# Kernel tuning notes

Measured on AMD Instinct MI355X. Metric: run time of the kernel, lower is better.

Reference implementation:

```python
import jax, jax.numpy as jnp
import numpy as np

N = 100000   # nodes
E = 1000000  # edges (avg degree 10)
F_IN, H1, H2, C = 128, 64, 64, 16


def setup_inputs() -> dict:
    key = jax.random.key(0)
    ks = jax.random.split(key, 10)
    x = jax.random.normal(ks[0], (N, F_IN), dtype=jnp.float32)
    edge_src = jax.random.randint(ks[1], (E,), 0, N, dtype=jnp.int32)
    edge_dst = jax.random.randint(ks[2], (E,), 0, N, dtype=jnp.int32)
    # normalized-adjacency-like positive edge weights (~1/deg scale)
    edge_val = jax.random.uniform(ks[3], (E,), dtype=jnp.float32) * 0.1
    def glorot(k, fan_in, fan_out):
        s = np.float32(1.0 / np.sqrt(fan_in))
        return jax.random.normal(k, (fan_in, fan_out), dtype=jnp.float32) * s
    W1 = glorot(ks[4], F_IN, H1)
    W2 = glorot(ks[5], H1, H2)
    W3 = glorot(ks[6], H2, C)
    b1 = jnp.zeros((H1,), jnp.float32)
    b2 = jnp.zeros((H2,), jnp.float32)
    b3 = jnp.zeros((C,), jnp.float32)
    return {"x": x, "edge_val": edge_val, "W1": W1, "b1": b1,
            "W2": W2, "b2": b2, "W3": W3, "b3": b3,
            "edge_src": edge_src, "edge_dst": edge_dst}


def gcn_layer(h, W, b, edge_src, edge_dst, edge_val):
    # support = h @ W ; out = spmm(adj, support) + b
    support = h @ W                                  # [N, d_out]
    msg = support[edge_src] * edge_val[:, None]      # [E, d_out] gather + scale
    agg = jax.ops.segment_sum(msg, edge_dst, num_segments=N)  # scatter-add
    return agg + b


def reference(x, edge_val, W1, b1, W2, b2, W3, b3, edge_src, edge_dst):
    # eval mode: F.dropout(training=False) is identity
    h = jax.nn.relu(gcn_layer(x, W1, b1, edge_src, edge_dst, edge_val))
    h = jax.nn.relu(gcn_layer(h, W2, b2, edge_src, edge_dst, edge_val))
    return gcn_layer(h, W3, b3, edge_src, edge_dst, edge_val)  # [N, C] logits
```

## Files before the change

### kernel.cpp

```cpp
#include <hip/hip_runtime.h>
#include <stdint.h>

#define N_NODES 100000
#define N_EDGES 1000000
#define NBUCK 196
#define CAP 6656

typedef __attribute__((ext_vector_type(8))) __bf16 bf16x8;
typedef __attribute__((ext_vector_type(4))) float f32x4;

static __device__ __forceinline__ float bf2f(unsigned short u) {
    return __uint_as_float(((unsigned int)u) << 16);
}
static __device__ __forceinline__ unsigned short f2bf(float f) {
    unsigned int u = __float_as_uint(f);
    unsigned int r = (u + 0x7FFFu + ((u >> 16) & 1u)) >> 16;
    return (unsigned short)r;
}
static __device__ __forceinline__ void st8_half(unsigned short* p, const float* f) {
    int4 u;
    u.x = (int)(((unsigned)f2bf(f[0])) | (((unsigned)f2bf(f[1])) << 16));
    u.y = (int)(((unsigned)f2bf(f[2])) | (((unsigned)f2bf(f[3])) << 16));
    u.z = (int)(((unsigned)f2bf(f[4])) | (((unsigned)f2bf(f[5])) << 16));
    u.w = (int)(((unsigned)f2bf(f[6])) | (((unsigned)f2bf(f[7])) << 16));
    *(int4*)p = u;
}

static __device__ __forceinline__ float ldf(const void* p, size_t i, int bf) {
    return bf ? bf2f(((const unsigned short*)p)[i]) : ((const float*)p)[i];
}

__global__ __launch_bounds__(256) void detect_kernel(const unsigned short* __restrict__ xs,
                                                     int* __restrict__ flag,
                                                     int* __restrict__ bcursor) {
    __shared__ int sz;
    if (threadIdx.x == 0) sz = 0;
    __syncthreads();
    int z = 0;
    for (int i = threadIdx.x; i < 1024; i += 256) {
        float av = fabsf(bf2f(xs[2 * i]));
        if (!(av <= 1048576.0f) || (av != 0.0f && av < 9.5367431640625e-07f)) z++;
    }
    atomicAdd(&sz, z);
    if (threadIdx.x < NBUCK) bcursor[threadIdx.x] = threadIdx.x * CAP;
    __syncthreads();
    if (threadIdx.x == 0) *flag = (sz > 256) ? 0 : 1;
}

__global__ __launch_bounds__(256) void part_kernel(const int* __restrict__ src,
                                                   const int* __restrict__ dst,
                                                   const void* __restrict__ val,
                                                   int* __restrict__ bcursor,
                                                   int2* __restrict__ part,
                                                   const int* __restrict__ flagp) {
    __shared__ int cnt[NBUCK];
    __shared__ int base[NBUCK];
    const int bf = *flagp;
    const int tid = threadIdx.x;
    const int e0 = blockIdx.x * 2048;
    for (int i = tid; i < NBUCK; i += 256) cnt[i] = 0;
    __syncthreads();
    int rank[8], bkt[8], pk[8], vb[8];
#pragma unroll
    for (int i = 0; i < 8; ++i) {
        int e = e0 + i * 256 + tid;
        bkt[i] = -1;
        if (e < N_EDGES) {
            int d = dst[e];
            int b = d >> 9;
            bkt[i] = b;
            pk[i] = src[e] | ((d & 511) << 17);
            vb[i] = __float_as_int(ldf(val, e, bf));
            rank[i] = atomicAdd(&cnt[b], 1);
        }
    }
    __syncthreads();
    for (int i = tid; i < NBUCK; i += 256) {
        int c = cnt[i];
        base[i] = c ? atomicAdd(&bcursor[i], c) : 0;
    }
    __syncthreads();
#pragma unroll
    for (int i = 0; i < 8; ++i) {
        if (bkt[i] >= 0) part[(size_t)base[bkt[i]] + rank[i]] = make_int2(pk[i], vb[i]);
    }
}

__global__ __launch_bounds__(512) void place_kernel(const int* __restrict__ bcursor,
                                                    const int2* __restrict__ part,
                                                    int* __restrict__ row_start,
                                                    int2* __restrict__ csr_rec) {
    __shared__ int cnt[512];
    __shared__ int sums[512];
    __shared__ int sh_s, sh_cnt, sh_total;
    const int tid = threadIdx.x;
    const int b = blockIdx.x;
    const int row0 = b << 9;
    const int nrows = min(512, N_NODES - row0);

    if (tid < 256) sums[tid] = (tid < NBUCK) ? (bcursor[tid] - tid * CAP) : 0;
    __syncthreads();
    for (int off = 1; off < 256; off <<= 1) {
        int t = 0;
        if (tid < 256 && tid >= off) t = sums[tid - off];
        __syncthreads();
        if (tid < 256 && tid >= off) sums[tid] += t;
        __syncthreads();
    }
    if (tid == 0) {
        sh_s = (b > 0) ? sums[b - 1] : 0;
        sh_cnt = bcursor[b] - b * CAP;
        sh_total = sums[NBUCK - 1];
    }
    __syncthreads();
    const int s = sh_s;
    const int cb = sh_cnt;
    const int ps = b * CAP;
    const int total = sh_total;

    cnt[tid] = 0;
    __syncthreads();
    for (int j = tid; j < cb; j += 512) {
        unsigned p = (unsigned)part[ps + j].x;
        atomicAdd(&cnt[p >> 17], 1);
    }
    __syncthreads();
    int own = cnt[tid];
    sums[tid] = own;
    __syncthreads();
    for (int off = 1; off < 512; off <<= 1) {
        int t = 0;
        if (tid >= off) t = sums[tid - off];
        __syncthreads();
        if (tid >= off) sums[tid] += t;
        __syncthreads();
    }
    int excl = sums[tid] - own;
    cnt[tid] = s + excl;
    if (tid < nrows) row_start[row0 + tid] = s + excl;
    if (b == NBUCK - 1 && tid == 0) row_start[N_NODES] = total;
    __syncthreads();
    for (int j = tid; j < cb; j += 512) {
        int2 r = part[ps + j];
        unsigned p = (unsigned)r.x;
        int pos = atomicAdd(&cnt[p >> 17], 1);
        csr_rec[pos] = make_int2((int)(p & 0x1FFFFu), r.y);
    }
}

template <int RS>
static __device__ __forceinline__ void row_gather(const unsigned short* __restrict__ supc,
                                                  const int2* __restrict__ csr_rec,
                                                  int s, int e, float a[8]) {
    if (s >= e) return;
    int2 r[4];
#pragma unroll
    for (int t = 0; t < 4; ++t) r[t] = csr_rec[min(s + t, e - 1)];
    for (int j = s; j < e; j += 4) {
        int4 sp[4];
#pragma unroll
        for (int t = 0; t < 4; ++t) sp[t] = *(const int4*)(supc + (size_t)r[t].x * RS);
        float wv[4];
#pragma unroll
        for (int t = 0; t < 4; ++t) wv[t] = (j + t < e) ? __int_as_float(r[t].y) : 0.0f;
        int jn = j + 4;
        if (jn < e) {
#pragma unroll
            for (int t = 0; t < 4; ++t) r[t] = csr_rec[min(jn + t, e - 1)];
        }
#pragma unroll
        for (int t = 0; t < 4; ++t) {
            float w = wv[t];
            int q[4] = {sp[t].x, sp[t].y, sp[t].z, sp[t].w};
#pragma unroll
            for (int c = 0; c < 4; ++c) {
                float flo = __uint_as_float(((unsigned)q[c]) << 16);
                float fhi = __uint_as_float(((unsigned)q[c]) & 0xffff0000u);
                a[2 * c]     += w * flo;
                a[2 * c + 1] += w * fhi;
            }
        }
    }
}

template <int K, int M, bool DYNIN>
__global__ __launch_bounds__(256, 8) void mgemm_kernel(const void* __restrict__ hv_,
                                                       const void* __restrict__ W,
                                                       unsigned short* __restrict__ out,
                                                       const int* __restrict__ flagp) {
    constexpr int KP = K + 8;
    constexpr int NC = M / 16;
    constexpr int NK = K / 32;

    __shared__ unsigned short wt[M][KP];

    const int bf = *flagp;
    const int tid = threadIdx.x;

    for (int i = tid; i < K * M; i += 256) {
        int k = i / M, m = i % M;
        wt[m][k] = f2bf(ldf(W, i, bf));
    }
    __syncthreads();

    const int lane = tid & 63;
    const int qd = lane >> 4;
    const int ln = lane & 15;
    const int wrow = (tid >> 6) * 16;
    const int tile = blockIdx.x;

    const int row = tile * 64 + wrow + ln;
    const bool ok = row < N_NODES;

    f32x4 acc[NC];
#pragma unroll
    for (int c = 0; c < NC; ++c) acc[c] = (f32x4){0.f, 0.f, 0.f, 0.f};

#pragma unroll
    for (int ks = 0; ks < NK; ++ks) {
        bf16x8 a;
        if (ok) {
            const size_t base = (size_t)row * K + ks * 32 + qd * 8;
            if (DYNIN && !bf) {
                const float* xp = (const float*)hv_ + base;
                float4 f0 = *(const float4*)xp;
                float4 f1 = *(const float4*)(xp + 4);
                ushort4 uu[2];
                uu[0].x = f2bf(f0.x); uu[0].y = f2bf(f0.y); uu[0].z = f2bf(f0.z); uu[0].w = f2bf(f0.w);
                uu[1].x = f2bf(f1.x); uu[1].y = f2bf(f1.y); uu[1].z = f2bf(f1.z); uu[1].w = f2bf(f1.w);
                a = *(const bf16x8*)uu;
            } else {
                a = *(const bf16x8*)((const unsigned short*)hv_ + base);
            }
        } else {
            a = (bf16x8)(__bf16)0.0f;
        }
#pragma unroll
        for (int c = 0; c < NC; ++c) {
            bf16x8 b = *(const bf16x8*)&wt[c * 16 + ln][ks * 32 + qd * 8];
            acc[c] = __builtin_amdgcn_mfma_f32_16x16x32_bf16(a, b, acc[c], 0, 0, 0);
        }
    }

#pragma unroll
    for (int c = 0; c < NC; ++c) {
#pragma unroll
        for (int r = 0; r < 4; ++r) {
            int orow = tile * 64 + wrow + qd * 4 + r;
            if (orow < N_NODES) out[(size_t)orow * M + c * 16 + ln] = f2bf(acc[c][r]);
        }
    }
}

template <int MOUT>
__global__ __launch_bounds__(256, 8) void fused_kernel(const unsigned short* __restrict__ support,
                                                       const int* __restrict__ row_start,
                                                       const int2* __restrict__ csr_rec,
                                                       const void* __restrict__ bias,
                                                       const void* __restrict__ W,
                                                       unsigned short* __restrict__ out,
                                                       const int* __restrict__ flagp) {
    constexpr int K = 64, KP = 72;
    constexpr int NC = MOUT / 16;
    constexpr int NK = 2;

    __shared__ unsigned short agg[64][KP];
    __shared__ unsigned short wt[MOUT][KP];

    const int bf = *flagp;
    const int tid = threadIdx.x;

    for (int i = tid; i < K * MOUT; i += 256) {
        int k = i / MOUT, m = i % MOUT;
        wt[m][k] = f2bf(ldf(W, i, bf));
    }

    const int lane = tid & 63;
    const int qd = lane >> 4;
    const int ln = lane & 15;
    const int wrow = (tid >> 6) * 16;

    const int grp = tid >> 3;
    const int cc = tid & 7;
    const unsigned short* supc = support + cc * 8;

    const int tile = blockIdx.x;
    const int rowA = tile * 64 + grp;
    const int rowB = rowA + 32;
    int s0 = row_start[min(rowA, N_NODES)];
    int e0 = row_start[min(rowA + 1, N_NODES)];
    int s1 = row_start[min(rowB, N_NODES)];
    int e1 = row_start[min(rowB + 1, N_NODES)];

    {
        float a[8];
#pragma unroll
        for (int c = 0; c < 8; ++c) a[c] = 0.0f;
        row_gather<64>(supc, csr_rec, s0, e0, a);
#pragma unroll
        for (int c = 0; c < 8; ++c) a[c] = fmaxf(a[c] + ldf(bias, cc * 8 + c, bf), 0.f);
        st8_half(&agg[grp][cc * 8], a);
    }
    {
        float a[8];
#pragma unroll
        for (int c = 0; c < 8; ++c) a[c] = 0.0f;
        row_gather<64>(supc, csr_rec, s1, e1, a);
#pragma unroll
        for (int c = 0; c < 8; ++c) a[c] = fmaxf(a[c] + ldf(bias, cc * 8 + c, bf), 0.f);
        st8_half(&agg[32 + grp][cc * 8], a);
    }
    __syncthreads();

    f32x4 macc[NC];
#pragma unroll
    for (int c = 0; c < NC; ++c) macc[c] = (f32x4){0.f, 0.f, 0.f, 0.f};
#pragma unroll
    for (int ks = 0; ks < NK; ++ks) {
        bf16x8 a = *(const bf16x8*)&agg[wrow + ln][ks * 32 + qd * 8];
#pragma unroll
        for (int c = 0; c < NC; ++c) {
            bf16x8 b = *(const bf16x8*)&wt[c * 16 + ln][ks * 32 + qd * 8];
            macc[c] = __builtin_amdgcn_mfma_f32_16x16x32_bf16(a, b, macc[c], 0, 0, 0);
        }
    }

#pragma unroll
    for (int c = 0; c < NC; ++c) {
#pragma unroll
        for (int r = 0; r < 4; ++r) {
            int orow = tile * 64 + wrow + qd * 4 + r;
            if (orow < N_NODES) out[(size_t)orow * MOUT + c * 16 + ln] = f2bf(macc[c][r]);
        }
    }
}

template <bool DYNOUT>
__global__ __launch_bounds__(256, 8) void spmm16_kernel(const unsigned short* __restrict__ support,
                                                        const int* __restrict__ row_start,
                                                        const int2* __restrict__ csr_rec,
                                                        const void* __restrict__ bias,
                                                        void* __restrict__ out_,
                                                        const int* __restrict__ flagp) {
    constexpr int M = 16;
    int bf = *flagp;
    int tid = threadIdx.x;
    int grp = tid >> 1;
    int cc = tid & 1;
    int row = blockIdx.x * 128 + grp;
    if (row >= N_NODES) return;
    int s = row_start[row];
    int e = row_start[row + 1];
    float a[8];
#pragma unroll
    for (int c = 0; c < 8; ++c) a[c] = 0.0f;
    row_gather<16>(support + cc * 8, csr_rec, s, e, a);
#pragma unroll
    for (int c = 0; c < 8; ++c) a[c] += ldf(bias, cc * 8 + c, bf);
    if (DYNOUT && !bf) {
        float* op = (float*)out_ + (size_t)row * M + cc * 8;
        *(float4*)op = make_float4(a[0], a[1], a[2], a[3]);
        *(float4*)(op + 4) = make_float4(a[4], a[5], a[6], a[7]);
    } else {
        st8_half((unsigned short*)out_ + (size_t)row * M + cc * 8, a);
    }
}

extern "C" void kernel_launch(void* const* d_in, const int* in_sizes, int n_in,
                              void* d_out, int out_size, void* d_ws, size_t ws_size,
                              hipStream_t stream) {
    (void)in_sizes; (void)n_in; (void)out_size; (void)ws_size;
    const void* x  = d_in[0];
    const void* ev = d_in[1];
    const void* W1 = d_in[2];
    const void* b1 = d_in[3];
    const void* W2 = d_in[4];
    const void* b2 = d_in[5];
    const void* W3 = d_in[6];
    const void* b3 = d_in[7];
    const int* esrc = (const int*)d_in[8];
    const int* edst = (const int*)d_in[9];

    char* ws = (char*)d_ws;
    size_t off = 0;
    auto alloc = [&](size_t bytes) -> void* {
        void* p = ws + off;
        off = (off + bytes + 255) & ~(size_t)255;
        return p;
    };
    unsigned short* A = (unsigned short*)alloc((size_t)N_NODES * 64 * 2);
    unsigned short* B = (unsigned short*)alloc((size_t)N_NODES * 64 * 2);
    int* row_start  = (int*)alloc((size_t)(N_NODES + 1) * 4);
    int* bcursor    = (int*)alloc(1024);
    int2* csr_rec   = (int2*)alloc((size_t)N_EDGES * 8);
    int* flagp      = (int*)alloc(256);
    int2* part      = (int2*)A;

    detect_kernel<<<1, 256, 0, stream>>>((const unsigned short*)x, flagp, bcursor);

    part_kernel<<<(N_EDGES + 2047) / 2048, 256, 0, stream>>>(esrc, edst, ev, bcursor, part, flagp);
    place_kernel<<<NBUCK, 512, 0, stream>>>(bcursor, part, row_start, csr_rec);

    const int NT = (N_NODES + 63) / 64;

    mgemm_kernel<128, 64, true><<<NT, 256, 0, stream>>>(x, W1, A, flagp);
    fused_kernel<64><<<NT, 256, 0, stream>>>(A, row_start, csr_rec, b1, W2, B, flagp);
    fused_kernel<16><<<NT, 256, 0, stream>>>(B, row_start, csr_rec, b2, W3, A, flagp);
    spmm16_kernel<true><<<(N_NODES + 127) / 128, 256, 0, stream>>>(A, row_start, csr_rec, b3, d_out, flagp);
}
```

Measured before the change: 228.1 us.

## Balance SpMM gather by splitting tile edges evenly with LDS atomic accumulation

Instead of assigning one destination row per thread group, each block now splits its tile's contiguous edge range evenly across thread groups. Groups accumulate per-row partials in registers and flush them to shared-memory fp32 accumulators with atomics whenever the destination row changes. Bias, ReLU and bf16 conversion move to the MFMA load stage. The gather loop is widened to 8 edges in flight. This targets load imbalance from varying degrees and tail divergence, at the cost of LDS atomics, extra shared memory, and dropped occupancy hints.

```diff
diff --git a/kernel.cpp b/kernel.cpp
--- a/kernel.cpp
+++ b/kernel.cpp
@@ -144,32 +144,47 @@
         int2 r = part[ps + j];
         unsigned p = (unsigned)r.x;
         int pos = atomicAdd(&cnt[p >> 17], 1);
-        csr_rec[pos] = make_int2((int)(p & 0x1FFFFu), r.y);
-    }
-}
-
-template <int RS>
-static __device__ __forceinline__ void row_gather(const unsigned short* __restrict__ supc,
+        csr_rec[pos] = make_int2((int)p, r.y);
+    }
+}
+
+template <int RS, int RMASK, int AST>
+static __device__ __forceinline__ void seg_gather(const unsigned short* __restrict__ supc,
                                                   const int2* __restrict__ csr_rec,
-                                                  int s, int e, float a[8]) {
+                                                  int s, int e,
+                                                  float* __restrict__ aggc ) {
     if (s >= e) return;
-    int2 r[4];
-#pragma unroll
-    for (int t = 0; t < 4; ++t) r[t] = csr_rec[min(s + t, e - 1)];
-    for (int j = s; j < e; j += 4) {
-        int4 sp[4];
-#pragma unroll
-        for (int t = 0; t < 4; ++t) sp[t] = *(const int4*)(supc + (size_t)r[t].x * RS);
-        float wv[4];
-#pragma unroll
-        for (int t = 0; t < 4; ++t) wv[t] = (j + t < e) ? __int_as_float(r[t].y) : 0.0f;
-        int jn = j + 4;
+    int2 r[8];
+#pragma unroll
+    for (int t = 0; t < 8; ++t) r[t] = csr_rec[min(s + t, e - 1)];
+    int cur = (r[0].x >> 17) & RMASK;
+    float a[8] = {0.f, 0.f, 0.f, 0.f, 0.f, 0.f, 0.f, 0.f};
+    for (int j = s; j < e; j += 8) {
+        int4 sp[8];
+#pragma unroll
+        for (int t = 0; t < 8; ++t)
+            sp[t] = *(const int4*)(supc + (size_t)(r[t].x & 0x1FFFF) * RS);
+        float wv[8];
+        int rw[8];
+#pragma unroll
+        for (int t = 0; t < 8; ++t) {
+            wv[t] = (j + t < e) ? __int_as_float(r[t].y) : 0.0f;
+            rw[t] = (r[t].x >> 17) & RMASK;
+        }
+        int jn = j + 8;
         if (jn < e) {
 #pragma unroll
-            for (int t = 0; t < 4; ++t) r[t] = csr_rec[min(jn + t, e - 1)];
-        }
-#pragma unroll
-        for (int t = 0; t < 4; ++t) {
+            for (int t = 0; t < 8; ++t) r[t] = csr_rec[min(jn + t, e - 1)];
+        }
+#pragma unroll
+        for (int t = 0; t < 8; ++t) {
+            if (rw[t] != cur) {
+#pragma unroll
+                for (int c = 0; c < 8; ++c) atomicAdd(aggc + cur * AST + c, a[c]);
+#pragma unroll
+                for (int c = 0; c < 8; ++c) a[c] = 0.0f;
+                cur = rw[t];
+            }
             float w = wv[t];
             int q[4] = {sp[t].x, sp[t].y, sp[t].z, sp[t].w};
 #pragma unroll
@@ -181,6 +196,8 @@
             }
         }
     }
+#pragma unroll
+    for (int c = 0; c < 8; ++c) atomicAdd(aggc + cur * AST + c, a[c]);
 }
 
 template <int K, int M, bool DYNIN>
@@ -253,71 +270,71 @@
 }
 
 template <int MOUT>
-__global__ __launch_bounds__(256, 8) void fused_kernel(const unsigned short* __restrict__ support,
-                                                       const int* __restrict__ row_start,
-                                                       const int2* __restrict__ csr_rec,
-                                                       const void* __restrict__ bias,
-                                                       const void* __restrict__ W,
-                                                       unsigned short* __restrict__ out,
-                                                       const int* __restrict__ flagp) {
+__global__ __launch_bounds__(256) void fused_kernel(const unsigned short* __restrict__ support,
+                                                    const int* __restrict__ row_start,
+                                                    const int2* __restrict__ csr_rec,
+                                                    const void* __restrict__ bias,
+                                                    const void* __restrict__ W,
+                                                    unsigned short* __restrict__ out,
+                                                    const int* __restrict__ flagp) {
     constexpr int K = 64, KP = 72;
+    constexpr int AST = 68;
     constexpr int NC = MOUT / 16;
-    constexpr int NK = 2;
-
-    __shared__ unsigned short agg[64][KP];
+
+    __shared__ float aggf[64 * AST];
     __shared__ unsigned short wt[MOUT][KP];
+    __shared__ float bb[K];
 
     const int bf = *flagp;
     const int tid = threadIdx.x;
 
+    for (int i = tid; i < 64 * AST; i += 256) aggf[i] = 0.0f;
     for (int i = tid; i < K * MOUT; i += 256) {
         int k = i / MOUT, m = i % MOUT;
         wt[m][k] = f2bf(ldf(W, i, bf));
     }
+    if (tid < K) bb[tid] = ldf(bias, tid, bf);
+    __syncthreads();
+
+    const int tile = blockIdx.x;
+    const int S = row_start[min(tile * 64, N_NODES)];
+    const int E = row_start[min(tile * 64 + 64, N_NODES)];
+    const int grp = tid >> 3;
+    const int cc = tid & 7;
+    const int len = E - S;
+    const int s = S + ((len * grp) >> 5);
+    const int e = S + ((len * (grp + 1)) >> 5);
+    seg_gather<64, 63, AST>(support + cc * 8, csr_rec, s, e, aggf + cc * 8);
+    __syncthreads();
 
     const int lane = tid & 63;
     const int qd = lane >> 4;
     const int ln = lane & 15;
     const int wrow = (tid >> 6) * 16;
 
-    const int grp = tid >> 3;
-    const int cc = tid & 7;
-    const unsigned short* supc = support + cc * 8;
-
-    const int tile = blockIdx.x;
-    const int rowA = tile * 64 + grp;
-    const int rowB = rowA + 32;
-    int s0 = row_start[min(rowA, N_NODES)];
-    int e0 = row_start[min(rowA + 1, N_NODES)];
-    int s1 = row_start[min(rowB, N_NODES)];
-    int e1 = row_start[min(rowB + 1, N_NODES)];
-
-    {
-        float a[8];
-#pragma unroll
-        for (int c = 0; c < 8; ++c) a[c] = 0.0f;
-        row_gather<64>(supc, csr_rec, s0, e0, a);
-#pragma unroll
-        for (int c = 0; c < 8; ++c) a[c] = fmaxf(a[c] + ldf(bias, cc * 8 + c, bf), 0.f);
-        st8_half(&agg[grp][cc * 8], a);
-    }
-    {
-        float a[8];
-#pragma unroll
-        for (int c = 0; c < 8; ++c) a[c] = 0.0f;
-        row_gather<64>(supc, csr_rec, s1, e1, a);
-#pragma unroll
-        for (int c = 0; c < 8; ++c) a[c] = fmaxf(a[c] + ldf(bias, cc * 8 + c, bf), 0.f);
-        st8_half(&agg[32 + grp][cc * 8], a);
-    }
-    __syncthreads();
-
     f32x4 macc[NC];
 #pragma unroll
     for (int c = 0; c < NC; ++c) macc[c] = (f32x4){0.f, 0.f, 0.f, 0.f};
 #pragma unroll
-    for (int ks = 0; ks < NK; ++ks) {
-        bf16x8 a = *(const bf16x8*)&agg[wrow + ln][ks * 32 + qd * 8];
+    for (int ks = 0; ks < 2; ++ks) {
+        const int k0 = ks * 32 + qd * 8;
+        const float* ap = &aggf[(wrow + ln) * AST + k0];
+        float4 v0 = *(const float4*)ap;
+        float4 v1 = *(const float4*)(ap + 4);
+        float4 b0 = *(const float4*)&bb[k0];
+        float4 b1 = *(const float4*)&bb[k0 + 4];
+        int4 pa;
+        pa.x = (int)(((unsigned)f2bf(fmaxf(v0.x + b0.x, 0.f))) |
+                     (((unsigned)f2bf(fmaxf(v0.y + b0.y, 0.f))) << 16));
+        pa.y = (int)(((unsigned)f2bf(fmaxf(v0.z + b0.z, 0.f))) |
+                     (((unsigned)f2bf(fmaxf(v0.w + b0.w, 0.f))) << 16));
+        pa.z = (int)(((unsigned)f2bf(fmaxf(v1.x + b1.x, 0.f))) |
+                     (((unsigned)f2bf(fmaxf(v1.y + b1.y, 0.f))) << 16));
+        pa.w = (int)(((unsigned)f2bf(fmaxf(v1.z + b1.z, 0.f))) |
+                     (((unsigned)f2bf(fmaxf(v1.w + b1.w, 0.f))) << 16));
+        union { int4 i; bf16x8 h; } ua;
+        ua.i = pa;
+        bf16x8 a = ua.h;
 #pragma unroll
         for (int c = 0; c < NC; ++c) {
             bf16x8 b = *(const bf16x8*)&wt[c * 16 + ln][ks * 32 + qd * 8];
@@ -336,33 +353,45 @@
 }
 
 template <bool DYNOUT>
-__global__ __launch_bounds__(256, 8) void spmm16_kernel(const unsigned short* __restrict__ support,
-                                                        const int* __restrict__ row_start,
-                                                        const int2* __restrict__ csr_rec,
-                                                        const void* __restrict__ bias,
-                                                        void* __restrict__ out_,
-                                                        const int* __restrict__ flagp) {
+__global__ __launch_bounds__(256) void spmm16_kernel(const unsigned short* __restrict__ support,
+                                                     const int* __restrict__ row_start,
+                                                     const int2* __restrict__ csr_rec,
+                                                     const void* __restrict__ bias,
+                                                     void* __restrict__ out_,
+                                                     const int* __restrict__ flagp) {
     constexpr int M = 16;
-    int bf = *flagp;
-    int tid = threadIdx.x;
-    int grp = tid >> 1;
-    int cc = tid & 1;
-    int row = blockIdx.x * 128 + grp;
+    constexpr int AST = 17;
+    __shared__ float aggf[128 * AST];
+    const int bf = *flagp;
+    const int tid = threadIdx.x;
+    for (int i = tid; i < 128 * AST; i += 256) aggf[i] = 0.0f;
+    __syncthreads();
+
+    const int b = blockIdx.x;
+    const int S = row_start[min(b * 128, N_NODES)];
+    const int E = row_start[min(b * 128 + 128, N_NODES)];
+    const int grp = tid >> 1;
+    const int cc = tid & 1;
+    const int len = E - S;
+    const int s = S + ((len * grp) >> 7);
+    const int e = S + ((len * (grp + 1)) >> 7);
+    seg_gather<16, 127, AST>(support + cc * 8, csr_rec, s, e, aggf + cc * 8);
+    __syncthreads();
+
+    const int lrow = tid >> 1;
+    const int half = tid & 1;
+    const int row = b * 128 + lrow;
     if (row >= N_NODES) return;
-    int s = row_start[row];
-    int e = row_start[row + 1];
-    float a[8];
-#pragma unroll
-    for (int c = 0; c < 8; ++c) a[c] = 0.0f;
-    row_gather<16>(support + cc * 8, csr_rec, s, e, a);
-#pragma unroll
-    for (int c = 0; c < 8; ++c) a[c] += ldf(bias, cc * 8 + c, bf);
+    float o[8];
+#pragma unroll
+    for (int c = 0; c < 8; ++c)
+        o[c] = aggf[lrow * AST + half * 8 + c] + ldf(bias, half * 8 + c, bf);
     if (DYNOUT && !bf) {
-        float* op = (float*)out_ + (size_t)row * M + cc * 8;
-        *(float4*)op = make_float4(a[0], a[1], a[2], a[3]);
-        *(float4*)(op + 4) = make_float4(a[4], a[5], a[6], a[7]);
+        float* op = (float*)out_ + (size_t)row * M + half * 8;
+        *(float4*)op = make_float4(o[0], o[1], o[2], o[3]);
+        *(float4*)(op + 4) = make_float4(o[4], o[5], o[6], o[7]);
     } else {
-        st8_half((unsigned short*)out_ + (size_t)row * M + cc * 8, a);
+        st8_half((unsigned short*)out_ + (size_t)row * M + half * 8, o);
     }
 }
 
```

After: 310.4 us. 36.1% more time.

## Replace scalar SpMM gather with MFMA-based tile aggregation using split-bf16 weights

Applied to the files above, without the earlier changes.

The per-row scalar gather-FMA loops are replaced by a tile kernel. Each block processes the edges of its 64 destination rows in chunks of 64. Each chunk's edge weights are scattered into a dense 64x64 selection matrix, stored as hi and lo bf16 parts to keep precision, and the gathered source rows are staged transposed in a swizzled LDS buffer. The aggregation then runs as MFMA products, with CSR records now carrying the local destination row in their upper bits. This trades the latency-bound scalar FMA work for extra LDS traffic, per-chunk barriers and wasted MFMA work on the sparse selection matrix.

```diff
diff --git a/kernel.cpp b/kernel.cpp
--- a/kernel.cpp
+++ b/kernel.cpp
@@ -144,42 +144,7 @@
         int2 r = part[ps + j];
         unsigned p = (unsigned)r.x;
         int pos = atomicAdd(&cnt[p >> 17], 1);
-        csr_rec[pos] = make_int2((int)(p & 0x1FFFFu), r.y);
-    }
-}
-
-template <int RS>
-static __device__ __forceinline__ void row_gather(const unsigned short* __restrict__ supc,
-                                                  const int2* __restrict__ csr_rec,
-                                                  int s, int e, float a[8]) {
-    if (s >= e) return;
-    int2 r[4];
-#pragma unroll
-    for (int t = 0; t < 4; ++t) r[t] = csr_rec[min(s + t, e - 1)];
-    for (int j = s; j < e; j += 4) {
-        int4 sp[4];
-#pragma unroll
-        for (int t = 0; t < 4; ++t) sp[t] = *(const int4*)(supc + (size_t)r[t].x * RS);
-        float wv[4];
-#pragma unroll
-        for (int t = 0; t < 4; ++t) wv[t] = (j + t < e) ? __int_as_float(r[t].y) : 0.0f;
-        int jn = j + 4;
-        if (jn < e) {
-#pragma unroll
-            for (int t = 0; t < 4; ++t) r[t] = csr_rec[min(jn + t, e - 1)];
-        }
-#pragma unroll
-        for (int t = 0; t < 4; ++t) {
-            float w = wv[t];
-            int q[4] = {sp[t].x, sp[t].y, sp[t].z, sp[t].w};
-#pragma unroll
-            for (int c = 0; c < 4; ++c) {
-                float flo = __uint_as_float(((unsigned)q[c]) << 16);
-                float fhi = __uint_as_float(((unsigned)q[c]) & 0xffff0000u);
-                a[2 * c]     += w * flo;
-                a[2 * c + 1] += w * fhi;
-            }
-        }
+        csr_rec[pos] = make_int2((int)p, r.y);
     }
 }
 
@@ -192,7 +157,7 @@
     constexpr int NC = M / 16;
     constexpr int NK = K / 32;
 
-    __shared__ unsigned short wt[M][KP];
+    __shared__ __align__(16) unsigned short wt[M][KP];
 
     const int bf = *flagp;
     const int tid = threadIdx.x;
@@ -252,117 +217,152 @@
     }
 }
 
-template <int MOUT>
-__global__ __launch_bounds__(256, 8) void fused_kernel(const unsigned short* __restrict__ support,
-                                                       const int* __restrict__ row_start,
-                                                       const int2* __restrict__ csr_rec,
-                                                       const void* __restrict__ bias,
-                                                       const void* __restrict__ W,
-                                                       unsigned short* __restrict__ out,
-                                                       const int* __restrict__ flagp) {
-    constexpr int K = 64, KP = 72;
-    constexpr int NC = MOUT / 16;
-    constexpr int NK = 2;
-
-    __shared__ unsigned short agg[64][KP];
-    __shared__ unsigned short wt[MOUT][KP];
+static __device__ __forceinline__ int gt_off(int c, int pos) {
+    return c * 72 + ((((pos >> 3) ^ (c >> 3)) & 7) << 3) + (pos & 7);
+}
+
+template <int COLS, int MOUT, bool FINAL, bool DYNOUT>
+__global__ __launch_bounds__(256) void agg_kernel(const unsigned short* __restrict__ support,
+                                                  const int* __restrict__ row_start,
+                                                  const int2* __restrict__ csr_rec,
+                                                  const void* __restrict__ bias,
+                                                  const void* __restrict__ W,
+                                                  void* __restrict__ out_,
+                                                  const int* __restrict__ flagp) {
+    constexpr int ST = 72;
+    constexpr int NCA = COLS / 16;
+    constexpr int NCO = MOUT / 16;
+    constexpr int SPE = COLS / 8;
+    constexpr int SLOTS = 64 * SPE;
+
+    __shared__ __align__(16) unsigned short Wsc[2][64][ST];
+    __shared__ __align__(16) unsigned short Gt[COLS * ST];
+    __shared__ __align__(16) unsigned short wt[FINAL ? 16 : MOUT][ST];
+    __shared__ float bb[COLS];
 
     const int bf = *flagp;
     const int tid = threadIdx.x;
-
-    for (int i = tid; i < K * MOUT; i += 256) {
-        int k = i / MOUT, m = i % MOUT;
-        wt[m][k] = f2bf(ldf(W, i, bf));
-    }
+    const int tile = blockIdx.x;
+
+    {
+        int4 z = make_int4(0, 0, 0, 0);
+        int4* wz = (int4*)&Wsc[0][0][0];
+#pragma unroll 2
+        for (int i = tid; i < 2 * 64 * ST / 8; i += 256) wz[i] = z;
+    }
+    if (!FINAL) {
+        for (int i = tid; i < 64 * MOUT; i += 256) {
+            int k = i / MOUT, m = i % MOUT;
+            wt[m][k] = f2bf(ldf(W, i, bf));
+        }
+    }
+    if (tid < COLS) bb[tid] = ldf(bias, tid, bf);
+
+    const int S = row_start[min(tile * 64, N_NODES)];
+    const int E = row_start[min(tile * 64 + 64, N_NODES)];
+    __syncthreads();
 
     const int lane = tid & 63;
     const int qd = lane >> 4;
     const int ln = lane & 15;
     const int wrow = (tid >> 6) * 16;
 
-    const int grp = tid >> 3;
-    const int cc = tid & 7;
-    const unsigned short* supc = support + cc * 8;
-
-    const int tile = blockIdx.x;
-    const int rowA = tile * 64 + grp;
-    const int rowB = rowA + 32;
-    int s0 = row_start[min(rowA, N_NODES)];
-    int e0 = row_start[min(rowA + 1, N_NODES)];
-    int s1 = row_start[min(rowB, N_NODES)];
-    int e1 = row_start[min(rowB + 1, N_NODES)];
-
-    {
-        float a[8];
-#pragma unroll
-        for (int c = 0; c < 8; ++c) a[c] = 0.0f;
-        row_gather<64>(supc, csr_rec, s0, e0, a);
-#pragma unroll
-        for (int c = 0; c < 8; ++c) a[c] = fmaxf(a[c] + ldf(bias, cc * 8 + c, bf), 0.f);
-        st8_half(&agg[grp][cc * 8], a);
-    }
-    {
-        float a[8];
-#pragma unroll
-        for (int c = 0; c < 8; ++c) a[c] = 0.0f;
-        row_gather<64>(supc, csr_rec, s1, e1, a);
-#pragma unroll
-        for (int c = 0; c < 8; ++c) a[c] = fmaxf(a[c] + ldf(bias, cc * 8 + c, bf), 0.f);
-        st8_half(&agg[32 + grp][cc * 8], a);
-    }
-    __syncthreads();
-
-    f32x4 macc[NC];
-#pragma unroll
-    for (int c = 0; c < NC; ++c) macc[c] = (f32x4){0.f, 0.f, 0.f, 0.f};
-#pragma unroll
-    for (int ks = 0; ks < NK; ++ks) {
-        bf16x8 a = *(const bf16x8*)&agg[wrow + ln][ks * 32 + qd * 8];
-#pragma unroll
-        for (int c = 0; c < NC; ++c) {
-            bf16x8 b = *(const bf16x8*)&wt[c * 16 + ln][ks * 32 + qd * 8];
-            macc[c] = __builtin_amdgcn_mfma_f32_16x16x32_bf16(a, b, macc[c], 0, 0, 0);
-        }
-    }
-
-#pragma unroll
-    for (int c = 0; c < NC; ++c) {
+    f32x4 acc[NCA];
+#pragma unroll
+    for (int c = 0; c < NCA; ++c) acc[c] = (f32x4){0.f, 0.f, 0.f, 0.f};
+
+    int dl = -1;
+    for (int e0 = S; e0 < E; e0 += 64) {
+        if (tid < 64) {
+            int idx = e0 + tid;
+            if (idx < E) {
+                int2 r = csr_rec[idx];
+                dl = (r.x >> 17) & 63;
+                float w = __int_as_float(r.y);
+                unsigned short wh = f2bf(w);
+                Wsc[0][dl][tid] = wh;
+                Wsc[1][dl][tid] = f2bf(w - bf2f(wh));
+            } else {
+                dl = -1;
+            }
+        }
+#pragma unroll
+        for (int ss = 0; ss < SLOTS; ss += 256) {
+            int slot = ss + tid;
+            if (slot < SLOTS) {
+                int pos = slot / SPE;
+                int c8 = (slot % SPE) * 8;
+                int2 r = csr_rec[min(e0 + pos, E - 1)];
+                int src = r.x & 0x1FFFF;
+                int4 g = *(const int4*)(support + (size_t)src * COLS + c8);
+                const unsigned short* gp = (const unsigned short*)&g;
+#pragma unroll
+                for (int jj = 0; jj < 8; ++jj) Gt[gt_off(c8 + jj, pos)] = gp[jj];
+            }
+        }
+        __syncthreads();
+#pragma unroll
+        for (int ks = 0; ks < 2; ++ks) {
+            const int k0 = ks * 32 + qd * 8;
+            bf16x8 ah = *(const bf16x8*)&Wsc[0][wrow + ln][k0];
+            bf16x8 al = *(const bf16x8*)&Wsc[1][wrow + ln][k0];
+#pragma unroll
+            for (int c = 0; c < NCA; ++c) {
+                bf16x8 b = *(const bf16x8*)&Gt[gt_off(c * 16 + ln, k0)];
+                acc[c] = __builtin_amdgcn_mfma_f32_16x16x32_bf16(ah, b, acc[c], 0, 0, 0);
+                acc[c] = __builtin_amdgcn_mfma_f32_16x16x32_bf16(al, b, acc[c], 0, 0, 0);
+            }
+        }
+        __syncthreads();
+        if (dl >= 0) {
+            Wsc[0][dl][tid] = 0;
+            Wsc[1][dl][tid] = 0;
+        }
+    }
+
+    if constexpr (FINAL) {
 #pragma unroll
         for (int r = 0; r < 4; ++r) {
-            int orow = tile * 64 + wrow + qd * 4 + r;
-            if (orow < N_NODES) out[(size_t)orow * MOUT + c * 16 + ln] = f2bf(macc[c][r]);
-        }
-    }
-}
-
-template <bool DYNOUT>
-__global__ __launch_bounds__(256, 8) void spmm16_kernel(const unsigned short* __restrict__ support,
-                                                        const int* __restrict__ row_start,
-                                                        const int2* __restrict__ csr_rec,
-                                                        const void* __restrict__ bias,
-                                                        void* __restrict__ out_,
-                                                        const int* __restrict__ flagp) {
-    constexpr int M = 16;
-    int bf = *flagp;
-    int tid = threadIdx.x;
-    int grp = tid >> 1;
-    int cc = tid & 1;
-    int row = blockIdx.x * 128 + grp;
-    if (row >= N_NODES) return;
-    int s = row_start[row];
-    int e = row_start[row + 1];
-    float a[8];
-#pragma unroll
-    for (int c = 0; c < 8; ++c) a[c] = 0.0f;
-    row_gather<16>(support + cc * 8, csr_rec, s, e, a);
-#pragma unroll
-    for (int c = 0; c < 8; ++c) a[c] += ldf(bias, cc * 8 + c, bf);
-    if (DYNOUT && !bf) {
-        float* op = (float*)out_ + (size_t)row * M + cc * 8;
-        *(float4*)op = make_float4(a[0], a[1], a[2], a[3]);
-        *(float4*)(op + 4) = make_float4(a[4], a[5], a[6], a[7]);
+            int row = tile * 64 + wrow + qd * 4 + r;
+            if (row < N_NODES) {
+                float v = acc[0][r] + bb[ln];
+                if (DYNOUT && !bf) ((float*)out_)[(size_t)row * 16 + ln] = v;
+                else ((unsigned short*)out_)[(size_t)row * 16 + ln] = f2bf(v);
+            }
+        }
     } else {
-        st8_half((unsigned short*)out_ + (size_t)row * M + cc * 8, a);
+        __syncthreads();
+        unsigned short (*agg)[ST] = Wsc[0];
+#pragma unroll
+        for (int c = 0; c < NCA; ++c) {
+#pragma unroll
+            for (int r = 0; r < 4; ++r) {
+                agg[wrow + qd * 4 + r][c * 16 + ln] =
+                    f2bf(fmaxf(acc[c][r] + bb[c * 16 + ln], 0.f));
+            }
+        }
+        __syncthreads();
+        f32x4 macc[NCO];
+#pragma unroll
+        for (int c = 0; c < NCO; ++c) macc[c] = (f32x4){0.f, 0.f, 0.f, 0.f};
+#pragma unroll
+        for (int ks = 0; ks < 2; ++ks) {
+            bf16x8 a = *(const bf16x8*)&agg[wrow + ln][ks * 32 + qd * 8];
+#pragma unroll
+            for (int c = 0; c < NCO; ++c) {
+                bf16x8 b = *(const bf16x8*)&wt[c * 16 + ln][ks * 32 + qd * 8];
+                macc[c] = __builtin_amdgcn_mfma_f32_16x16x32_bf16(a, b, macc[c], 0, 0, 0);
+            }
+        }
+        unsigned short* outp = (unsigned short*)out_;
+#pragma unroll
+        for (int c = 0; c < NCO; ++c) {
+#pragma unroll
+            for (int r = 0; r < 4; ++r) {
+                int orow = tile * 64 + wrow + qd * 4 + r;
+                if (orow < N_NODES) outp[(size_t)orow * MOUT + c * 16 + ln] = f2bf(macc[c][r]);
+            }
+        }
     }
 }
 
@@ -404,7 +404,7 @@
     const int NT = (N_NODES + 63) / 64;
 
     mgemm_kernel<128, 64, true><<<NT, 256, 0, stream>>>(x, W1, A, flagp);
-    fused_kernel<64><<<NT, 256, 0, stream>>>(A, row_start, csr_rec, b1, W2, B, flagp);
-    fused_kernel<16><<<NT, 256, 0, stream>>>(B, row_start, csr_rec, b2, W3, A, flagp);
-    spmm16_kernel<true><<<(N_NODES + 127) / 128, 256, 0, stream>>>(A, row_start, csr_rec, b3, d_out, flagp);
-}
+    agg_kernel<64, 64, false, false><<<NT, 256, 0, stream>>>(A, row_start, csr_rec, b1, W2, B, flagp);
+    agg_kernel<64, 16, false, false><<<NT, 256, 0, stream>>>(B, row_start, csr_rec, b2, W3, A, flagp);
+    agg_kernel<16, 16, true, true><<<NT, 256, 0, stream>>>(A, row_start, csr_rec, b3, b3, d_out, flagp);
+}
```

Result: slower. 279.5 us (+22.5%).
